# Kernel tuning notes

Hardware: AMD Instinct MI355X
Metric: run time of the kernel (lower is better)

The kernel has to match this reference:

```python
import jax, jax.numpy as jnp
import numpy as np

B, T = 128, 1024
H1, H2 = 768, 768


def setup_inputs() -> dict:
    key = jax.random.key(0)
    ks = jax.random.split(key, 12)
    s1 = 1.0 / np.sqrt(H1)
    s2 = 1.0 / np.sqrt(H2)
    return {
        "x": jax.random.normal(ks[0], (B, 2, T), dtype=jnp.float32),
        "W_ih1": jax.random.uniform(ks[1], (H1, 2), jnp.float32, -s1, s1),
        "W_hh1": jax.random.uniform(ks[2], (H1, H1), jnp.float32, -s1, s1),
        "b_ih1": jax.random.uniform(ks[3], (H1,), jnp.float32, -s1, s1),
        "b_hh1": jax.random.uniform(ks[4], (H1,), jnp.float32, -s1, s1),
        "W_ih2": jax.random.uniform(ks[5], (H2, H1), jnp.float32, -s2, s2),
        "W_hh2": jax.random.uniform(ks[6], (H2, H2), jnp.float32, -s2, s2),
        "b_ih2": jax.random.uniform(ks[7], (H2,), jnp.float32, -s2, s2),
        "b_hh2": jax.random.uniform(ks[8], (H2,), jnp.float32, -s2, s2),
        "W_lin": jax.random.uniform(ks[9], (2, H2), jnp.float32, -s2, s2),
        "b_lin": jax.random.uniform(ks[10], (2,), jnp.float32, -s2, s2),
        "future": 0,
    }


def reference(x, W_ih1, W_hh1, b_ih1, b_hh1, W_ih2, W_hh2, b_ih2, b_hh2,
              W_lin, b_lin, future):
    Bb = x.shape[0]
    xs = jnp.transpose(x, (2, 0, 1))  # [T, B, 2]

    def cell(xt, ht, W_ih, W_hh, b_ih, b_hh):
        return jnp.tanh(xt @ W_ih.T + b_ih + ht @ W_hh.T + b_hh)

    def step(carry, xt):
        h1, h2 = carry
        h1 = cell(xt, h1, W_ih1, W_hh1, b_ih1, b_hh1)
        h2 = cell(h1, h2, W_ih2, W_hh2, b_ih2, b_hh2)
        out = h2 @ W_lin.T + b_lin  # [B, 2]
        return (h1, h2), out

    h1 = jnp.zeros((Bb, W_hh1.shape[0]), dtype=x.dtype)
    h2 = jnp.zeros((Bb, W_hh2.shape[0]), dtype=x.dtype)
    (h1, h2), outs = jax.lax.scan(step, (h1, h2), xs)  # outs: [T, B, 2]

    if future > 0:
        def fstep(carry, _):
            h1, h2, out = carry
            h1 = cell(out, h1, W_ih1, W_hh1, b_ih1, b_hh1)
            h2 = cell(h1, h2, W_ih2, W_hh2, b_ih2, b_hh2)
            out = h2 @ W_lin.T + b_lin
            return (h1, h2, out), out
        _, fouts = jax.lax.scan(fstep, (h1, h2, outs[-1]), None, length=future)
        outs = jnp.concatenate([outs, fouts], axis=0)

    return jnp.transpose(outs, (1, 2, 0))  # [B, 2, T+future]
```

## Files before the change

kernel.cpp:

```cpp
#include <hip/hip_runtime.h>
#include <math.h>


typedef short s16x8 __attribute__((ext_vector_type(8)));
typedef float fx4   __attribute__((ext_vector_type(4)));

#define NWG    256
#define T_LEN  1024
#define H      768
#define GROUPS 8
#define GROWS  16

#define MAP_OFF    0
#define KBR_OFF    1024
#define GRP_BASE   8192
#define G_FL1 0
#define G_FH2 128
#define G_EL1 256
#define G_EH2 768
#define G_PB  2048
#define G_H1  16384
#define G_H2  212992
#define GRP_STRIDE 315392
#define HB_SZ 24576
#define WS_TOTAL (GRP_BASE + GROUPS * GRP_STRIDE)

__device__ __forceinline__ unsigned short f2bf(float x) {
    unsigned u = __float_as_uint(x);
    unsigned r = (u + 0x7FFFu + ((u >> 16) & 1u)) >> 16;
    return (unsigned short)r;
}
__device__ __forceinline__ float bf2f(unsigned short b) {
    return __uint_as_float(((unsigned)b) << 16);
}
__device__ __forceinline__ fx4 mfma16(s16x8 a, s16x8 b, fx4 c) {
    return __builtin_amdgcn_mfma_f32_16x16x32_bf16(a, b, c, 0, 0, 0);
}

__device__ __forceinline__ void st_ag(unsigned* p, unsigned v) {
    __hip_atomic_store(p, v, __ATOMIC_RELAXED, __HIP_MEMORY_SCOPE_AGENT);
}
__device__ __forceinline__ unsigned ld_ag(const unsigned* p) {
    return __hip_atomic_load(p, __ATOMIC_RELAXED, __HIP_MEMORY_SCOPE_AGENT);
}
__device__ __forceinline__ void acq_ag() {
    __builtin_amdgcn_fence(__ATOMIC_ACQUIRE, "agent");
}
__device__ __forceinline__ void st32_sc0(unsigned* p, unsigned v) {
    asm volatile("global_store_dword %0, %1, off sc0" :: "v"(p), "v"(v) : "memory");
}
__device__ __forceinline__ void stflag_l2(unsigned* p, unsigned v) {
    asm volatile("global_atomic_swap %0, %1, off" :: "v"(p), "v"(v) : "memory");
}
__device__ __forceinline__ void umax_l2(unsigned* p, unsigned v) {
    asm volatile("global_atomic_umax %0, %1, off" :: "v"(p), "v"(v) : "memory");
}
__device__ __forceinline__ unsigned rdflag_l2(unsigned* p) {
    unsigned v, z = 0;
    asm volatile("global_atomic_add %0, %1, %2, off sc0\n\ts_waitcnt vmcnt(0)"
                 : "=v"(v) : "v"(p), "v"(z) : "memory");
    return v;
}
__device__ __forceinline__ void inv_l1() {
    asm volatile("buffer_inv sc0" ::: "memory");
}

template<bool LOCAL> __device__ __forceinline__ unsigned rdp(unsigned* p) {
    if constexpr (LOCAL) return rdflag_l2(p); else return ld_ag(p);
}
template<bool LOCAL> __device__ __forceinline__ void std32(unsigned* p, unsigned v) {
    if constexpr (LOCAL) st32_sc0(p, v); else st_ag(p, v);
}

__device__ __forceinline__ void load_wfrag(const float* __restrict__ W,
                                           int col, int kk, s16x8& hi, s16x8& lo) {
    const float* p = W + (long)col * H + kk;
#pragma unroll
    for (int j = 0; j < 8; j++) {
        float w = p[j];
        unsigned short h = f2bf(w);
        float r = w - bf2f(h);
        hi[j] = (short)h;
        lo[j] = (short)f2bf(r);
    }
}

__device__ __forceinline__ void ld6(const unsigned short* p, s16x8 (&d)[6]) {
#pragma unroll
    for (int ks = 0; ks < 6; ks++)
        d[ks] = *reinterpret_cast<const s16x8*>(p + ks * 32);
}

__device__ __forceinline__ unsigned wave_min(unsigned v) {
#pragma unroll
    for (int o = 32; o; o >>= 1) {
        unsigned u = (unsigned)__shfl_xor((int)v, o);
        v = v < u ? v : u;
    }
    return v;
}

__device__ __forceinline__ void arrive_pub(unsigned* own, unsigned ownval,
                                           unsigned* raw, int n, int ownidx,
                                           unsigned* reps, int tid) {
    if (tid == 0) stflag_l2(own, ownval);
    if (tid < 64) {
        asm volatile("s_waitcnt vmcnt(0)" ::: "memory");
        unsigned v = 0xFFFFFFFFu;
        if (tid < n) v = (tid == ownidx) ? ownval : rdflag_l2(raw + tid);
        unsigned m = wave_min(v);
        if (m >= ownval && tid < 8) umax_l2(reps + tid * 16, m);
    }
}

__device__ __forceinline__ unsigned wait_ep(unsigned* reps, unsigned* raw, int n,
                                            unsigned T, int tid, int lrank,
                                            unsigned cached, bool do_inv,
                                            volatile unsigned* sh) {
    if (cached < T) {
        if (tid < 64) {
            unsigned* myrep = reps + (lrank & 7) * 16;
            unsigned m = 0;
            long spin = 0;
            for (;;) {
                if ((spin & 7) == 7) {
                    unsigned v = (tid < n) ? rdflag_l2(raw + tid) : 0xFFFFFFFFu;
                    m = wave_min(v);
                } else {
                    if (tid == 0) m = rdflag_l2(myrep);
                    m = (unsigned)__shfl((int)m, 0);
                }
                if (m >= T) break;
                __builtin_amdgcn_s_sleep(1);
                if (++spin > (1L << 20)) break;
            }
            if (tid == 0) *sh = m;
        }
    }
    if (do_inv && tid == 0) inv_l1();
    __syncthreads();
    return (cached < T) ? *sh : cached;
}

__device__ __forceinline__ void wait_agent(unsigned* f, int n, unsigned T,
                                           int tid, bool acquire) {
    if (tid < 64) {
        int l = tid < n ? tid : n - 1;
        long spin = 0;
        for (;;) {
            if (wave_min(ld_ag(f + l)) >= T) break;
            __builtin_amdgcn_s_sleep(1);
            if (++spin > (1L << 20)) break;
        }
    }
    if (acquire && tid == 0) acq_ag();
    __syncthreads();
}

#define DRAIN() do { asm volatile("s_waitcnt vmcnt(0)" ::: "memory"); __syncthreads(); } while (0)

template<bool LOCAL>
__device__ __forceinline__ void run_group(
    int group, int lrank, int tid, int lane, int w, int l15, int lk8,
    const float* __restrict__ x,
    const float* __restrict__ Wih1, const float* __restrict__ Whh1,
    const float* __restrict__ bih1, const float* __restrict__ bhh1,
    const float* __restrict__ Wih2, const float* __restrict__ Whh2,
    const float* __restrict__ bih2, const float* __restrict__ bhh2,
    const float* __restrict__ Wlin, const float* __restrict__ blin,
    float* __restrict__ out, unsigned char* __restrict__ gb,
    float (*red)[16][97], volatile unsigned* shm)
{
    unsigned* fL1 = (unsigned*)(gb + G_FL1);
    unsigned* fH2 = (unsigned*)(gb + G_FH2);
    unsigned* eL1 = (unsigned*)(gb + G_EL1);
    unsigned* eH2 = (unsigned*)(gb + G_EH2);
    float*    Pb  = (float*)(gb + G_PB);
    const int kb0 = w * 192;

    if (lrank < 8) {
        const int c = lrank;
        const int col0 = c * 96;

        s16x8 whi[6][6], wlo[6][6];
#pragma unroll
        for (int ks = 0; ks < 6; ks++)
#pragma unroll
            for (int nt = 0; nt < 6; nt++)
                load_wfrag(Whh1, col0 + nt * 16 + l15, kb0 + ks * 32 + lk8,
                           whi[ks][nt], wlo[ks][nt]);

        const int er = tid >> 4;
        const int ec0 = (tid & 15) * 6;
        const int b = group * GROWS + er;
        float bs[6], wi0[6], wi1[6];
#pragma unroll
        for (int j = 0; j < 6; j++) {
            int cg = col0 + ec0 + j;
            bs[j] = bih1[cg] + bhh1[cg];
            wi0[j] = Wih1[cg * 2 + 0];
            wi1[j] = Wih1[cg * 2 + 1];
        }
        const int ov = tid >> 5;
        const int oj = tid & 31;
        const int orow = 2 * c + (ov >> 1);
        const int ooo = ov & 1;
        const float blv = blin[ooo];

        unsigned fh2c = 0, fl1c = 0;

        for (int t = 0; t < T_LEN; t++) {
            const int rs = (t + 3) & 3;
            const int wsl = t & 3;
            float x0 = x[b * 2048 + t];
            float x1 = x[b * 2048 + 1024 + t];

            if (t >= 3) {
                if constexpr (LOCAL)
                    fh2c = wait_ep(eH2, fH2, 24, (unsigned)(t - 2), tid, lrank, fh2c, false, &shm[0]);
                else
                    wait_agent(fH2, 24, (unsigned)(t - 2), tid, false);
                if (tid < 128) {
                    float p = 0.f;
                    if (oj < 24)
                        p = __uint_as_float(rdp<LOCAL>((unsigned*)
                            (Pb + ((((t - 3) & 3) * 16 + orow) * 2 + ooo) * 24 + oj)));
#pragma unroll
                    for (int o = 16; o; o >>= 1) p += __shfl_down(p, o, 32);
                    if (oj == 0) out[(group * GROWS + orow) * 2048 + ooo * 1024 + (t - 3)] = p + blv;
                }
            }

            if (t) {
                if constexpr (LOCAL)
                    fl1c = wait_ep(eL1, fL1, 8, (unsigned)t, tid, lrank, fl1c, true, &shm[1]);
                else
                    wait_agent(fL1, 8, (unsigned)t, tid, true);
            }

            const unsigned short* Hh = (const unsigned short*)(gb + G_H1 + rs * 2 * HB_SZ);
            const unsigned short* Hl = (const unsigned short*)(gb + G_H1 + rs * 2 * HB_SZ + HB_SZ);
            s16x8 ah[6], al[6];
            ld6(Hh + l15 * H + kb0 + lk8, ah);
            ld6(Hl + l15 * H + kb0 + lk8, al);

            fx4 acc[6];
#pragma unroll
            for (int nt = 0; nt < 6; nt++) acc[nt] = fx4{0.f, 0.f, 0.f, 0.f};
#pragma unroll
            for (int ks = 0; ks < 6; ks++)
#pragma unroll
                for (int nt = 0; nt < 6; nt++) {
                    acc[nt] = mfma16(ah[ks], whi[ks][nt], acc[nt]);
                    acc[nt] = mfma16(ah[ks], wlo[ks][nt], acc[nt]);
                    acc[nt] = mfma16(al[ks], whi[ks][nt], acc[nt]);
                }

#pragma unroll
            for (int nt = 0; nt < 6; nt++)
#pragma unroll
                for (int i = 0; i < 4; i++)
                    red[w][(lane >> 4) * 4 + i][nt * 16 + l15] = acc[nt][i];
            __syncthreads();

            unsigned hw[3], lw[3];
#pragma unroll
            for (int jj = 0; jj < 3; jj++) {
                unsigned hp = 0, lp = 0;
#pragma unroll
                for (int k = 0; k < 2; k++) {
                    int j = jj * 2 + k;
                    int cc = ec0 + j;
                    float v = red[0][er][cc] + red[1][er][cc] + red[2][er][cc] + red[3][er][cc];
                    v += x0 * wi0[j] + x1 * wi1[j] + bs[j];
                    v = tanhf(v);
                    unsigned short hb = f2bf(v);
                    unsigned short lb = f2bf(v - bf2f(hb));
                    hp |= ((unsigned)hb) << (16 * k);
                    lp |= ((unsigned)lb) << (16 * k);
                }
                hw[jj] = hp; lw[jj] = lp;
            }

            unsigned* Dh = (unsigned*)(gb + G_H1 + wsl * 2 * HB_SZ) + ((long)er * H + col0 + ec0) / 2;
            unsigned* Dl = (unsigned*)(gb + G_H1 + wsl * 2 * HB_SZ + HB_SZ) + ((long)er * H + col0 + ec0) / 2;
            std32<LOCAL>(Dh + 0, hw[0]); std32<LOCAL>(Dh + 1, hw[1]); std32<LOCAL>(Dh + 2, hw[2]);
            std32<LOCAL>(Dl + 0, lw[0]); std32<LOCAL>(Dl + 1, lw[1]); std32<LOCAL>(Dl + 2, lw[2]);

            DRAIN();
            if constexpr (LOCAL)
                arrive_pub(fL1 + c, (unsigned)(t + 1), fL1, 8, c, eL1, tid);
            else if (tid == 0)
                st_ag(fL1 + c, (unsigned)(t + 1));
        }

        if constexpr (LOCAL)
            fh2c = wait_ep(eH2, fH2, 24, (unsigned)T_LEN, tid, lrank, fh2c, false, &shm[0]);
        else
            wait_agent(fH2, 24, (unsigned)T_LEN, tid, false);
        if (tid < 128) {
#pragma unroll
            for (int par = 0; par < 3; par++) {
                int tt = T_LEN - 3 + par;
                float p = 0.f;
                if (oj < 24)
                    p = __uint_as_float(rdp<LOCAL>((unsigned*)
                        (Pb + (((tt & 3) * 16 + orow) * 2 + ooo) * 24 + oj)));
#pragma unroll
                for (int o = 16; o; o >>= 1) p += __shfl_down(p, o, 32);
                if (oj == 0) out[(group * GROWS + orow) * 2048 + ooo * 1024 + tt] = p + blv;
            }
        }
    } else {
        const int q = lrank - 8;
        const int col0 = q * 32;

        s16x8 ghi[2][6], glo[2][6], ihi[2][6], ilo[2][6];
#pragma unroll
        for (int nt = 0; nt < 2; nt++)
#pragma unroll
            for (int ks = 0; ks < 6; ks++) {
                load_wfrag(Whh2, col0 + nt * 16 + l15, kb0 + ks * 32 + lk8, ghi[nt][ks], glo[nt][ks]);
                load_wfrag(Wih2, col0 + nt * 16 + l15, kb0 + ks * 32 + lk8, ihi[nt][ks], ilo[nt][ks]);
            }

        const int er = tid >> 4;
        const int ec0 = (tid & 15) * 2;
        const float bsA = bih2[col0 + ec0] + bhh2[col0 + ec0];
        const float bsB = bih2[col0 + ec0 + 1] + bhh2[col0 + ec0 + 1];

        const int ro = tid >> 1, oo = tid & 1;
        float wl[32];
        if (tid < 32) {
#pragma unroll
            for (int cc = 0; cc < 32; cc++) wl[cc] = Wlin[oo * H + col0 + cc];
        }

        unsigned fh2c = 0, fl1c = 0;

        for (int t = 0; t < T_LEN; t++) {
            const int rb = (t + 1) & 1;
            const int wb = t & 1;
            const int hs = t & 3;

            if (t) {
                if constexpr (LOCAL)
                    fh2c = wait_ep(eH2, fH2, 24, (unsigned)t, tid, lrank, fh2c, true, &shm[2]);
                else
                    wait_agent(fH2, 24, (unsigned)t, tid, true);
            }

            const unsigned short* Gh = (const unsigned short*)(gb + G_H2 + rb * 2 * HB_SZ);
            const unsigned short* Gl = (const unsigned short*)(gb + G_H2 + rb * 2 * HB_SZ + HB_SZ);
            s16x8 ah[6], al[6];
            ld6(Gh + l15 * H + kb0 + lk8, ah);
            ld6(Gl + l15 * H + kb0 + lk8, al);

            fx4 a2[2];
            a2[0] = fx4{0.f, 0.f, 0.f, 0.f};
            a2[1] = fx4{0.f, 0.f, 0.f, 0.f};
#pragma unroll
            for (int ks = 0; ks < 6; ks++)
#pragma unroll
                for (int nt = 0; nt < 2; nt++) {
                    a2[nt] = mfma16(ah[ks], ghi[nt][ks], a2[nt]);
                    a2[nt] = mfma16(ah[ks], glo[nt][ks], a2[nt]);
                    a2[nt] = mfma16(al[ks], ghi[nt][ks], a2[nt]);
                }

            if constexpr (LOCAL)
                fl1c = wait_ep(eL1, fL1, 8, (unsigned)(t + 1), tid, lrank, fl1c, true, &shm[3]);
            else
                wait_agent(fL1, 8, (unsigned)(t + 1), tid, true);

            const unsigned short* Hh = (const unsigned short*)(gb + G_H1 + hs * 2 * HB_SZ);
            const unsigned short* Hl = (const unsigned short*)(gb + G_H1 + hs * 2 * HB_SZ + HB_SZ);
            ld6(Hh + l15 * H + kb0 + lk8, ah);
            ld6(Hl + l15 * H + kb0 + lk8, al);
#pragma unroll
            for (int ks = 0; ks < 6; ks++)
#pragma unroll
                for (int nt = 0; nt < 2; nt++) {
                    a2[nt] = mfma16(ah[ks], ihi[nt][ks], a2[nt]);
                    a2[nt] = mfma16(ah[ks], ilo[nt][ks], a2[nt]);
                    a2[nt] = mfma16(al[ks], ihi[nt][ks], a2[nt]);
                }

#pragma unroll
            for (int nt = 0; nt < 2; nt++)
#pragma unroll
                for (int i = 0; i < 4; i++)
                    red[w][(lane >> 4) * 4 + i][nt * 16 + l15] = a2[nt][i];
            __syncthreads();

            float v0 = red[0][er][ec0] + red[1][er][ec0] + red[2][er][ec0] + red[3][er][ec0] + bsA;
            float v1 = red[0][er][ec0 + 1] + red[1][er][ec0 + 1] + red[2][er][ec0 + 1] + red[3][er][ec0 + 1] + bsB;
            v0 = tanhf(v0); v1 = tanhf(v1);
            unsigned short hb0 = f2bf(v0), hb1 = f2bf(v1);
            unsigned hp = ((unsigned)hb0) | (((unsigned)hb1) << 16);
            unsigned lp = ((unsigned)f2bf(v0 - bf2f(hb0))) | (((unsigned)f2bf(v1 - bf2f(hb1))) << 16);
            unsigned* Dh = (unsigned*)(gb + G_H2 + wb * 2 * HB_SZ) + ((long)er * H + col0 + ec0) / 2;
            unsigned* Dl = (unsigned*)(gb + G_H2 + wb * 2 * HB_SZ + HB_SZ) + ((long)er * H + col0 + ec0) / 2;
            std32<LOCAL>(Dh, hp);
            std32<LOCAL>(Dl, lp);
            red[0][er][ec0] = v0;
            red[0][er][ec0 + 1] = v1;
            __syncthreads();

            if (tid < 32) {
                float s = 0.f;
#pragma unroll
                for (int cc = 0; cc < 32; cc++) s += red[0][ro][cc] * wl[cc];
                std32<LOCAL>((unsigned*)&Pb[(((t & 3) * 16 + ro) * 2 + oo) * 24 + q],
                             __float_as_uint(s));
            }

            DRAIN();
            if constexpr (LOCAL)
                arrive_pub(fH2 + q, (unsigned)(t + 1), fH2, 24, q, eH2, tid);
            else if (tid == 0)
                st_ag(fH2 + q, (unsigned)(t + 1));
        }
    }
}

__global__ __launch_bounds__(256, 1) void rnn_persist(
    const float* __restrict__ x,
    const float* __restrict__ Wih1, const float* __restrict__ Whh1,
    const float* __restrict__ bih1, const float* __restrict__ bhh1,
    const float* __restrict__ Wih2, const float* __restrict__ Whh2,
    const float* __restrict__ bih2, const float* __restrict__ bhh2,
    const float* __restrict__ Wlin, const float* __restrict__ blin,
    float* __restrict__ out, unsigned char* __restrict__ ws)
{
    const int wg = blockIdx.x;
    const int tid = threadIdx.x;
    const int lane = tid & 63;
    const int w = tid >> 6;
    const int l15 = lane & 15;
    const int lk8 = (lane >> 4) * 8;

    __shared__ float red[4][16][97];
    __shared__ int iscr[256];
    __shared__ unsigned shm[4];

    unsigned* map = (unsigned*)(ws + MAP_OFF);
    unsigned* kbr = (unsigned*)(ws + KBR_OFF);

    int key;
    asm volatile("s_getreg_b32 %0, hwreg(HW_REG_XCC_ID, 0, 4)" : "=s"(key));
    key &= 0xF;

    if (tid == 0) st_ag(map + wg, (unsigned)(key + 1));
    unsigned kj;
    {
        long spin = 0;
        for (;;) {
            kj = ld_ag(map + tid);
            if (kj) break;
            __builtin_amdgcn_s_sleep(2);
            if (++spin > (1L << 20)) break;
        }
    }
    int contrib = (((int)kj - 1) < key || (((int)kj - 1) == key && tid < wg)) ? 1 : 0;
    iscr[tid] = contrib;
    __syncthreads();
#pragma unroll
    for (int s = 128; s; s >>= 1) {
        if (tid < s) iscr[tid] += iscr[tid + s];
        __syncthreads();
    }
    const int rank = iscr[0];
    __syncthreads();
    const int group = rank >> 5, lrank = rank & 31;

    if (tid == 0) st_ag(kbr + rank, (unsigned)(key + 1));
    unsigned kv;
    {
        long spin = 0;
        for (;;) {
            kv = ld_ag(kbr + tid);
            if (kv) break;
            __builtin_amdgcn_s_sleep(2);
            if (++spin > (1L << 20)) break;
        }
    }
    int eq = ((int)kv - 1 == key) ? 1 : 0;
    int bad = ((tid >> 5) == group && !eq) ? 1 : 0;
    iscr[tid] = eq | (bad << 16);
    __syncthreads();
#pragma unroll
    for (int s = 128; s; s >>= 1) {
        if (tid < s) iscr[tid] += iscr[tid + s];
        __syncthreads();
    }
    const int r0 = iscr[0];
    __syncthreads();
    const bool local = ((r0 & 0xFFFF) == 32) && ((r0 >> 16) == 0);

    unsigned char* gb = ws + GRP_BASE + (size_t)group * GRP_STRIDE;

    if (local)
        run_group<true>(group, lrank, tid, lane, w, l15, lk8,
                        x, Wih1, Whh1, bih1, bhh1, Wih2, Whh2, bih2, bhh2,
                        Wlin, blin, out, gb, red, shm);
    else
        run_group<false>(group, lrank, tid, lane, w, l15, lk8,
                         x, Wih1, Whh1, bih1, bhh1, Wih2, Whh2, bih2, bhh2,
                         Wlin, blin, out, gb, red, shm);
}

extern "C" void kernel_launch(void* const* d_in, const int* in_sizes, int n_in,
                              void* d_out, int out_size, void* d_ws, size_t ws_size,
                              hipStream_t stream) {
    const float* x    = (const float*)d_in[0];
    const float* Wih1 = (const float*)d_in[1];
    const float* Whh1 = (const float*)d_in[2];
    const float* bih1 = (const float*)d_in[3];
    const float* bhh1 = (const float*)d_in[4];
    const float* Wih2 = (const float*)d_in[5];
    const float* Whh2 = (const float*)d_in[6];
    const float* bih2 = (const float*)d_in[7];
    const float* bhh2 = (const float*)d_in[8];
    const float* Wlin = (const float*)d_in[9];
    const float* blin = (const float*)d_in[10];

    hipMemsetAsync(d_ws, 0, WS_TOTAL, stream);

    rnn_persist<<<NWG, 256, 0, stream>>>(x, Wih1, Whh1, bih1, bhh1,
                                         Wih2, Whh2, bih2, bhh2,
                                         Wlin, blin, (float*)d_out,
                                         (unsigned char*)d_ws);
}
```

Measured before the change: 6.462 ms.

## Replace publisher-side epoch aggregation with collector-based subscriber replica flags

```diff
diff --git a/kernel.cpp b/kernel.cpp
--- a/kernel.cpp
+++ b/kernel.cpp
@@ -16,11 +16,11 @@
 #define GRP_BASE   8192
 #define G_FL1 0
 #define G_FH2 128
-#define G_EL1 256
-#define G_EH2 768
-#define G_PB  2048
-#define G_H1  16384
-#define G_H2  212992
+#define G_EL1 512
+#define G_EH2 2560
+#define G_PB  4608
+#define G_H1  20480
+#define G_H2  217088
 #define GRP_STRIDE 315392
 #define HB_SZ 24576
 #define WS_TOTAL (GRP_BASE + GROUPS * GRP_STRIDE)
@@ -100,30 +100,41 @@
     return v;
 }
 
-__device__ __forceinline__ void arrive_pub(unsigned* own, unsigned ownval,
-                                           unsigned* raw, int n, int ownidx,
-                                           unsigned* reps, int tid) {
-    if (tid == 0) stflag_l2(own, ownval);
-    if (tid < 64) {
-        asm volatile("s_waitcnt vmcnt(0)" ::: "memory");
-        unsigned v = 0xFFFFFFFFu;
-        if (tid < n) v = (tid == ownidx) ? ownval : rdflag_l2(raw + tid);
-        unsigned m = wave_min(v);
-        if (m >= ownval && tid < 8) umax_l2(reps + tid * 16, m);
-    }
-}
-
-__device__ __forceinline__ unsigned wait_ep(unsigned* reps, unsigned* raw, int n,
-                                            unsigned T, int tid, int lrank,
-                                            unsigned cached, bool do_inv,
-                                            volatile unsigned* sh) {
+__device__ __forceinline__ unsigned wait_col(unsigned* raw, int n, unsigned T,
+                                             int tid, unsigned* reps,
+                                             unsigned cached, bool do_inv,
+                                             volatile unsigned* sh) {
     if (cached < T) {
         if (tid < 64) {
-            unsigned* myrep = reps + (lrank & 7) * 16;
+            unsigned m;
+            long spin = 0;
+            for (;;) {
+                unsigned v = (tid < n) ? rdflag_l2(raw + tid) : 0xFFFFFFFFu;
+                m = wave_min(v);
+                if (m >= T) break;
+                __builtin_amdgcn_s_sleep(1);
+                if (++spin > (1L << 20)) break;
+            }
+            if (tid < 32) umax_l2(reps + tid * 16, m);
+            if (tid == 0) *sh = m;
+        }
+    }
+    if (do_inv && tid == 0) inv_l1();
+    __syncthreads();
+    return (cached < T) ? *sh : cached;
+}
+
+__device__ __forceinline__ unsigned wait_sub(unsigned* reps, unsigned* raw, int n,
+                                             unsigned T, int tid, int lrank,
+                                             unsigned cached, bool do_inv,
+                                             volatile unsigned* sh) {
+    if (cached < T) {
+        if (tid < 64) {
+            unsigned* myrep = reps + lrank * 16;
             unsigned m = 0;
             long spin = 0;
             for (;;) {
-                if ((spin & 7) == 7) {
+                if ((spin & 63) == 63) {
                     unsigned v = (tid < n) ? rdflag_l2(raw + tid) : 0xFFFFFFFFu;
                     m = wave_min(v);
                 } else {
@@ -217,7 +228,7 @@
 
             if (t >= 3) {
                 if constexpr (LOCAL)
-                    fh2c = wait_ep(eH2, fH2, 24, (unsigned)(t - 2), tid, lrank, fh2c, false, &shm[0]);
+                    fh2c = wait_sub(eH2, fH2, 24, (unsigned)(t - 2), tid, lrank, fh2c, false, &shm[0]);
                 else
                     wait_agent(fH2, 24, (unsigned)(t - 2), tid, false);
                 if (tid < 128) {
@@ -232,10 +243,14 @@
             }
 
             if (t) {
-                if constexpr (LOCAL)
-                    fl1c = wait_ep(eL1, fL1, 8, (unsigned)t, tid, lrank, fl1c, true, &shm[1]);
-                else
+                if constexpr (LOCAL) {
+                    if (c == 0)
+                        fl1c = wait_col(fL1, 8, (unsigned)t, tid, eL1, fl1c, true, &shm[1]);
+                    else
+                        fl1c = wait_sub(eL1, fL1, 8, (unsigned)t, tid, lrank, fl1c, true, &shm[1]);
+                } else {
                     wait_agent(fL1, 8, (unsigned)t, tid, true);
+                }
             }
 
             const unsigned short* Hh = (const unsigned short*)(gb + G_H1 + rs * 2 * HB_SZ);
@@ -288,14 +303,14 @@
             std32<LOCAL>(Dl + 0, lw[0]); std32<LOCAL>(Dl + 1, lw[1]); std32<LOCAL>(Dl + 2, lw[2]);
 
             DRAIN();
-            if constexpr (LOCAL)
-                arrive_pub(fL1 + c, (unsigned)(t + 1), fL1, 8, c, eL1, tid);
-            else if (tid == 0)
-                st_ag(fL1 + c, (unsigned)(t + 1));
+            if (tid == 0) {
+                if constexpr (LOCAL) stflag_l2(fL1 + c, (unsigned)(t + 1));
+                else st_ag(fL1 + c, (unsigned)(t + 1));
+            }
         }
 
         if constexpr (LOCAL)
-            fh2c = wait_ep(eH2, fH2, 24, (unsigned)T_LEN, tid, lrank, fh2c, false, &shm[0]);
+            fh2c = wait_col(fH2, 24, (unsigned)T_LEN, tid, eH2, fh2c, false, &shm[0]);
         else
             wait_agent(fH2, 24, (unsigned)T_LEN, tid, false);
         if (tid < 128) {
@@ -344,10 +359,14 @@
             const int hs = t & 3;
 
             if (t) {
-                if constexpr (LOCAL)
-                    fh2c = wait_ep(eH2, fH2, 24, (unsigned)t, tid, lrank, fh2c, true, &shm[2]);
-                else
+                if constexpr (LOCAL) {
+                    if (q == 0)
+                        fh2c = wait_col(fH2, 24, (unsigned)t, tid, eH2, fh2c, true, &shm[2]);
+                    else
+                        fh2c = wait_sub(eH2, fH2, 24, (unsigned)t, tid, lrank, fh2c, true, &shm[2]);
+                } else {
                     wait_agent(fH2, 24, (unsigned)t, tid, true);
+                }
             }
 
             const unsigned short* Gh = (const unsigned short*)(gb + G_H2 + rb * 2 * HB_SZ);
@@ -369,7 +388,7 @@
                 }
 
             if constexpr (LOCAL)
-                fl1c = wait_ep(eL1, fL1, 8, (unsigned)(t + 1), tid, lrank, fl1c, true, &shm[3]);
+                fl1c = wait_sub(eL1, fL1, 8, (unsigned)(t + 1), tid, lrank, fl1c, true, &shm[3]);
             else
                 wait_agent(fL1, 8, (unsigned)(t + 1), tid, true);
 
@@ -416,10 +435,10 @@
             }
 
             DRAIN();
-            if constexpr (LOCAL)
-                arrive_pub(fH2 + q, (unsigned)(t + 1), fH2, 24, q, eH2, tid);
-            else if (tid == 0)
-                st_ag(fH2 + q, (unsigned)(t + 1));
+            if (tid == 0) {
+                if constexpr (LOCAL) stflag_l2(fH2 + q, (unsigned)(t + 1));
+                else st_ag(fH2 + q, (unsigned)(t + 1));
+            }
         }
     }
 }
```

After: 6.714 ms. +3.9%, slower.

## Split layer-2 hidden-state and projection flags; prefetch h1 when already ready

Applied to the files above, without the earlier changes.

```diff
diff --git a/kernel.cpp b/kernel.cpp
--- a/kernel.cpp
+++ b/kernel.cpp
@@ -14,13 +14,14 @@
 #define MAP_OFF    0
 #define KBR_OFF    1024
 #define GRP_BASE   8192
-#define G_FL1 0
-#define G_FH2 128
-#define G_EL1 256
-#define G_EH2 768
-#define G_PB  2048
-#define G_H1  16384
-#define G_H2  212992
+#define G_FL1  0
+#define G_FH2D 128
+#define G_FP   256
+#define G_EL1  512
+#define G_EH2D 2560
+#define G_PB   4608
+#define G_H1   20480
+#define G_H2   217088
 #define GRP_STRIDE 315392
 #define HB_SZ 24576
 #define WS_TOTAL (GRP_BASE + GROUPS * GRP_STRIDE)
@@ -109,7 +110,7 @@
         unsigned v = 0xFFFFFFFFu;
         if (tid < n) v = (tid == ownidx) ? ownval : rdflag_l2(raw + tid);
         unsigned m = wave_min(v);
-        if (m >= ownval && tid < 8) umax_l2(reps + tid * 16, m);
+        if (m >= ownval && tid < 32) umax_l2(reps + tid * 16, m);
     }
 }
 
@@ -119,7 +120,7 @@
                                             volatile unsigned* sh) {
     if (cached < T) {
         if (tid < 64) {
-            unsigned* myrep = reps + (lrank & 7) * 16;
+            unsigned* myrep = reps + lrank * 16;
             unsigned m = 0;
             long spin = 0;
             for (;;) {
@@ -142,6 +143,27 @@
     return (cached < T) ? *sh : cached;
 }
 
+__device__ __forceinline__ unsigned wait_raw(unsigned* raw, int n, unsigned T,
+                                             int tid, unsigned cached,
+                                             volatile unsigned* sh) {
+    if (cached < T) {
+        if (tid < 64) {
+            unsigned m;
+            long spin = 0;
+            for (;;) {
+                unsigned v = (tid < n) ? rdflag_l2(raw + tid) : 0xFFFFFFFFu;
+                m = wave_min(v);
+                if (m >= T) break;
+                __builtin_amdgcn_s_sleep(1);
+                if (++spin > (1L << 20)) break;
+            }
+            if (tid == 0) *sh = m;
+        }
+    }
+    __syncthreads();
+    return (cached < T) ? *sh : cached;
+}
+
 __device__ __forceinline__ void wait_agent(unsigned* f, int n, unsigned T,
                                            int tid, bool acquire) {
     if (tid < 64) {
@@ -171,11 +193,12 @@
     float* __restrict__ out, unsigned char* __restrict__ gb,
     float (*red)[16][97], volatile unsigned* shm)
 {
-    unsigned* fL1 = (unsigned*)(gb + G_FL1);
-    unsigned* fH2 = (unsigned*)(gb + G_FH2);
-    unsigned* eL1 = (unsigned*)(gb + G_EL1);
-    unsigned* eH2 = (unsigned*)(gb + G_EH2);
-    float*    Pb  = (float*)(gb + G_PB);
+    unsigned* fL1  = (unsigned*)(gb + G_FL1);
+    unsigned* fH2d = (unsigned*)(gb + G_FH2D);
+    unsigned* fP   = (unsigned*)(gb + G_FP);
+    unsigned* eL1  = (unsigned*)(gb + G_EL1);
+    unsigned* eH2d = (unsigned*)(gb + G_EH2D);
+    float*    Pb   = (float*)(gb + G_PB);
     const int kb0 = w * 192;
 
     if (lrank < 8) {
@@ -207,7 +230,7 @@
         const int ooo = ov & 1;
         const float blv = blin[ooo];
 
-        unsigned fh2c = 0, fl1c = 0;
+        unsigned fpc = 0, fl1c = 0;
 
         for (int t = 0; t < T_LEN; t++) {
             const int rs = (t + 3) & 3;
@@ -217,9 +240,9 @@
 
             if (t >= 3) {
                 if constexpr (LOCAL)
-                    fh2c = wait_ep(eH2, fH2, 24, (unsigned)(t - 2), tid, lrank, fh2c, false, &shm[0]);
+                    fpc = wait_raw(fP, 24, (unsigned)(t - 2), tid, fpc, &shm[0]);
                 else
-                    wait_agent(fH2, 24, (unsigned)(t - 2), tid, false);
+                    wait_agent(fP, 24, (unsigned)(t - 2), tid, false);
                 if (tid < 128) {
                     float p = 0.f;
                     if (oj < 24)
@@ -295,9 +318,9 @@
         }
 
         if constexpr (LOCAL)
-            fh2c = wait_ep(eH2, fH2, 24, (unsigned)T_LEN, tid, lrank, fh2c, false, &shm[0]);
+            fpc = wait_raw(fP, 24, (unsigned)T_LEN, tid, fpc, &shm[0]);
         else
-            wait_agent(fH2, 24, (unsigned)T_LEN, tid, false);
+            wait_agent(fP, 24, (unsigned)T_LEN, tid, false);
         if (tid < 128) {
 #pragma unroll
             for (int par = 0; par < 3; par++) {
@@ -345,16 +368,26 @@
 
             if (t) {
                 if constexpr (LOCAL)
-                    fh2c = wait_ep(eH2, fH2, 24, (unsigned)t, tid, lrank, fh2c, true, &shm[2]);
+                    fh2c = wait_ep(eH2d, fH2d, 24, (unsigned)t, tid, lrank, fh2c, true, &shm[2]);
                 else
-                    wait_agent(fH2, 24, (unsigned)t, tid, true);
+                    wait_agent(fH2d, 24, (unsigned)t, tid, true);
             }
 
             const unsigned short* Gh = (const unsigned short*)(gb + G_H2 + rb * 2 * HB_SZ);
             const unsigned short* Gl = (const unsigned short*)(gb + G_H2 + rb * 2 * HB_SZ + HB_SZ);
-            s16x8 ah[6], al[6];
+            const unsigned short* Hh = (const unsigned short*)(gb + G_H1 + hs * 2 * HB_SZ);
+            const unsigned short* Hl = (const unsigned short*)(gb + G_H1 + hs * 2 * HB_SZ + HB_SZ);
+
+            s16x8 ah[6], al[6], bh[6], bl[6];
+            bool h1rdy = false;
+            if constexpr (LOCAL) h1rdy = (fl1c >= (unsigned)(t + 1));
+
             ld6(Gh + l15 * H + kb0 + lk8, ah);
             ld6(Gl + l15 * H + kb0 + lk8, al);
+            if (h1rdy) {
+                ld6(Hh + l15 * H + kb0 + lk8, bh);
+                ld6(Hl + l15 * H + kb0 + lk8, bl);
+            }
 
             fx4 a2[2];
             a2[0] = fx4{0.f, 0.f, 0.f, 0.f};
@@ -368,22 +401,22 @@
                     a2[nt] = mfma16(al[ks], ghi[nt][ks], a2[nt]);
                 }
 
-            if constexpr (LOCAL)
-                fl1c = wait_ep(eL1, fL1, 8, (unsigned)(t + 1), tid, lrank, fl1c, true, &shm[3]);
-            else
-                wait_agent(fL1, 8, (unsigned)(t + 1), tid, true);
-
-            const unsigned short* Hh = (const unsigned short*)(gb + G_H1 + hs * 2 * HB_SZ);
-            const unsigned short* Hl = (const unsigned short*)(gb + G_H1 + hs * 2 * HB_SZ + HB_SZ);
-            ld6(Hh + l15 * H + kb0 + lk8, ah);
-            ld6(Hl + l15 * H + kb0 + lk8, al);
+            if (!h1rdy) {
+                if constexpr (LOCAL)
+                    fl1c = wait_ep(eL1, fL1, 8, (unsigned)(t + 1), tid, lrank, fl1c, false, &shm[3]);
+                else
+                    wait_agent(fL1, 8, (unsigned)(t + 1), tid, true);
+                ld6(Hh + l15 * H + kb0 + lk8, bh);
+                ld6(Hl + l15 * H + kb0 + lk8, bl);
+            }
+
 #pragma unroll
             for (int ks = 0; ks < 6; ks++)
 #pragma unroll
                 for (int nt = 0; nt < 2; nt++) {
-                    a2[nt] = mfma16(ah[ks], ihi[nt][ks], a2[nt]);
-                    a2[nt] = mfma16(ah[ks], ilo[nt][ks], a2[nt]);
-                    a2[nt] = mfma16(al[ks], ihi[nt][ks], a2[nt]);
+                    a2[nt] = mfma16(bh[ks], ihi[nt][ks], a2[nt]);
+                    a2[nt] = mfma16(bh[ks], ilo[nt][ks], a2[nt]);
+                    a2[nt] = mfma16(bl[ks], ihi[nt][ks], a2[nt]);
                 }
 
 #pragma unroll
@@ -405,7 +438,12 @@
             std32<LOCAL>(Dl, lp);
             red[0][er][ec0] = v0;
             red[0][er][ec0 + 1] = v1;
-            __syncthreads();
+
+            DRAIN();
+            if constexpr (LOCAL)
+                arrive_pub(fH2d + q, (unsigned)(t + 1), fH2d, 24, q, eH2d, tid);
+            else if (tid == 0)
+                st_ag(fH2d + q, (unsigned)(t + 1));
 
             if (tid < 32) {
                 float s = 0.f;
@@ -416,10 +454,10 @@
             }
 
             DRAIN();
-            if constexpr (LOCAL)
-                arrive_pub(fH2 + q, (unsigned)(t + 1), fH2, 24, q, eH2, tid);
-            else if (tid == 0)
-                st_ag(fH2 + q, (unsigned)(t + 1));
+            if (tid == 0) {
+                if constexpr (LOCAL) stflag_l2(fP + q, (unsigned)(t + 1));
+                else st_ag(fP + q, (unsigned)(t + 1));
+            }
         }
     }
 }
```

After: 6.473 ms. Within noise of the previous version (+0.2%).
